# Kernel tuning notes

Hardware: AMD Instinct MI355X
Metric: run time of the kernel (lower is better)

The kernel has to match this reference:

```python
import jax, jax.numpy as jnp
import numpy as np

IN_FEATURES = 1024
OUT_FEATURES = 256
NUM_KNOTS = 10
SPLINE_ORDER = 3
NUM_BASIS = NUM_KNOTS + SPLINE_ORDER  # 13
EPS = 1e-8


def setup_inputs() -> dict:
    key = jax.random.key(0)
    k1, k2 = jax.random.split(key)
    x = jax.random.normal(k1, (8192, IN_FEATURES), dtype=jnp.float32)
    spline_coeffs = jax.random.normal(
        k2, (OUT_FEATURES, IN_FEATURES, NUM_BASIS), dtype=jnp.float32) * 0.1
    knots = jnp.linspace(-1.0, 1.0, NUM_KNOTS + 2 * SPLINE_ORDER, dtype=jnp.float32)
    return {"x": x, "spline_coeffs": spline_coeffs, "knots": knots}


def _basis_functions(x, knots):
    # x: (B, I) already tanh-normalized; returns (B, I, NUM_BASIS)
    xc = jnp.clip(x, -1.0, 1.0)[..., None]          # (B, I, 1)
    left = knots[:NUM_BASIS - 1]                     # (nb-1,)
    center = knots[1:NUM_BASIS]                      # (nb-1,)
    right = knots[2:NUM_BASIS + 1]                   # (nb-1,)  (i+2 < len(knots) always)
    mask_l = (xc >= left) & (xc < center)
    mask_r = (xc >= center) & (xc < right)
    up = mask_l.astype(xc.dtype) * (xc - left) / (center - left + EPS)
    down = mask_r.astype(xc.dtype) * (right - xc) / (right - center + EPS)
    b = up + down                                    # (B, I, nb-1)
    # last basis column is never written in the original loop -> zeros
    return jnp.pad(b, ((0, 0), (0, 0), (0, 1)))


def reference(x, spline_coeffs, knots):
    x_norm = jnp.tanh(x)
    basis = _basis_functions(x_norm, knots)          # (B, I, K)
    # output[b, j] = sum_i sum_k basis[b, i, k] * coeffs[j, i, k]
    return jnp.einsum('bik,jik->bj', basis, spline_coeffs)
```

## Files before the change

### kernel.cpp

```cpp
#include <hip/hip_runtime.h>
#include <cstdint>
#include <cstddef>


typedef _Float16 half2_v __attribute__((ext_vector_type(2)));
typedef __fp16  fp16x2  __attribute__((ext_vector_type(2)));
typedef _Float16 f16x8 __attribute__((ext_vector_type(8)));
typedef float f32x4 __attribute__((ext_vector_type(4)));

__device__ __forceinline__ half2_v u32_as_h2(uint32_t u) {
  union { uint32_t u; half2_v h; } c; c.u = u; return c.h;
}
__device__ __forceinline__ uint32_t h2_as_u32(half2_v h) {
  union { uint32_t u; half2_v h; } c; c.h = h; return c.u;
}
__device__ __forceinline__ half2_v cvt_pk_h2(float a, float b) {
  union { fp16x2 f; half2_v h; } c;
  c.f = __builtin_amdgcn_cvt_pkrtz(a, b);
  return c.h;
}
__device__ __forceinline__ float dot2f(half2_v a, half2_v b, float c) {
#if __has_builtin(__builtin_amdgcn_fdot2)
  return __builtin_amdgcn_fdot2(a, b, c, false);
#else
  return c + (float)a[0] * (float)b[0] + (float)a[1] * (float)b[1];
#endif
}
__device__ __forceinline__ uint16_t f16_bits(float v) {
  union { _Float16 h; uint16_t u; } c; c.h = (_Float16)v; return c.u;
}

__device__ __forceinline__ float fast_tanhf(float v) {
  const float e = __expf(2.0f * v);
  return 1.0f - 2.0f / (e + 1.0f);
}

#define KSTEP 0.13333333333333333f
#define KINV  7.49999943750004f
__device__ __forceinline__ void kan_weights(float xin, float& w0, float& w1, int& lo) {
  float xc = fast_tanhf(xin);
  xc = fminf(fmaxf(xc, -1.0f), 1.0f);
  int m = (int)((xc + 1.0f) * 7.5f);
  m = min(max(m, 0), 14);
  const float k0 = fmaf((float)m, KSTEP, -1.0f);
  const float up = (xc - k0) * KINV;
  const float dn = (k0 + KSTEP - xc) * KINV;
  w0 = (m == 0) ? up : ((m <= 12) ? dn : 0.0f);
  w1 = (m >= 1 && m <= 11) ? up : 0.0f;
  lo = min(max(m - 1, 0), 11);
}

__device__ __forceinline__ void load_lds16(const void* g, void* l) {
  __builtin_amdgcn_global_load_lds((const __attribute__((address_space(1))) void*)g,
                                   (__attribute__((address_space(3))) void*)l, 16, 0, 0);
}

#define GMM 8192
#define GNN 256
#define KI  16
#define GK2 (1024 * KI)
#define KSPL2 8
#define IPER (1024 / KSPL2)
#define BM2 128
#define BN2 256
#define NGRAN 64
#define NBODY 16

__global__ __launch_bounds__(256)
void kan_prep_B2(const float* __restrict__ coef, uint32_t* __restrict__ B2,
                 float4* __restrict__ outz) {
  const int tid = blockIdx.x * 256 + threadIdx.x;
  const float* cp = coef + (size_t)tid * 13;
  uint32_t w[8];
#pragma unroll
  for (int q = 0; q < 6; ++q) w[q] = h2_as_u32(cvt_pk_h2(cp[2 * q], cp[2 * q + 1]));
  w[6] = 0u; w[7] = 0u;
  uint4* p = (uint4*)(B2 + (size_t)tid * 8);
  p[0] = make_uint4(w[0], w[1], w[2], w[3]);
  p[1] = make_uint4(w[4], w[5], w[6], w[7]);
  const float4 z = make_float4(0.f, 0.f, 0.f, 0.f);
  outz[tid] = z;
  outz[tid + 262144] = z;
}

__global__ __launch_bounds__(512, 4)
void kan_gemm10(const float* __restrict__ x, const _Float16* __restrict__ B2,
                float* __restrict__ out) {
  __shared__ __align__(16) char Bs[4][16384];
  __shared__ __align__(16) char As[2][8192];
  char* BsP = (char*)Bs;
  char* AsP = (char*)As;

  const int t    = threadIdx.x;
  const int lane = t & 63;
  const int wv   = t >> 6;
  const int wm   = (wv & 1) * 64;
  const int wn   = (wv >> 1) * 64;
  const int fr   = lane & 15;
  const int fq   = lane >> 4;
  const int m0   = blockIdx.z * BM2;
  const int i00  = blockIdx.x * IPER;

  const int fr_swz = (((wm >> 2) + (fr >> 2)) & 1) * 16;
  const int a_base = (wm + fr) * 32 + (((fq & 1) * 16) ^ fr_swz) + (fq >> 1) * 4096;
  const int b_base = (wn + fr) * 64 + ((fq ^ (fr & 3)) * 16);

  f32x4 acc[4][4];
#pragma unroll
  for (int a = 0; a < 4; ++a)
#pragma unroll
    for (int b = 0; b < 4; ++b) acc[a][b] = (f32x4){0.f, 0.f, 0.f, 0.f};

  const int srow0 = t >> 2, sc0 = t & 3;
  const int srow1 = 128 + (t >> 2);
  const _Float16* sp0 = B2 + (size_t)srow0 * GK2 + (size_t)i00 * KI
                        + ((sc0 ^ (srow0 & 3)) * 8);
  const _Float16* sp1 = B2 + (size_t)srow1 * GK2 + (size_t)i00 * KI
                        + ((sc0 ^ (srow1 & 3)) * 8);
  const int xrow   = (t >> 1) & 127;
  const int parity = t & 1;
  const int i_off  = (t >> 8) & 1;
  const float* xptr = x + (size_t)(m0 + xrow) * 1024 + i00 + 2 * parity + i_off;
  const int exp_off = (i_off * 128 + xrow) * 32;
  const int p_swz   = ((xrow >> 2) & 1) * 16;

  auto expand1 = [&](int aw, float xv) {
    float w0, w1; int lo;
    kan_weights(xv, w0, w1, lo);
    const uint32_t wp  = (uint32_t)f16_bits(w0) | ((uint32_t)f16_bits(w1) << 16);
    const uint32_t wlo = (lo & 1) ? (wp << 16) : wp;
    const uint32_t whi = (lo & 1) ? (wp >> 16) : 0u;
    const int w = lo >> 1;
    char* rb = AsP + aw + exp_off;
    *(uint4*)(rb + p_swz)        = make_uint4(0u, 0u, 0u, 0u);
    *(uint4*)(rb + (p_swz ^ 16)) = make_uint4(0u, 0u, 0u, 0u);
    *(uint32_t*)(rb + (((w + 1) * 4) ^ p_swz)) = whi;
    *(uint32_t*)(rb + ((w * 4) ^ p_swz))       = wlo;
  };

  float xa, xb, xn1, xn2;

  xa = xptr[0];
  xb = xptr[4];
  load_lds16(sp0, BsP + 0 + t * 16);
  load_lds16(sp1, BsP + 0 + 8192 + t * 16);
  sp0 += 32; sp1 += 32;
  load_lds16(sp0, BsP + 16384 + t * 16);
  load_lds16(sp1, BsP + 16384 + 8192 + t * 16);
  sp0 += 32; sp1 += 32;
  if (parity == 0) expand1(0, xa);
  asm volatile("s_waitcnt vmcnt(2) lgkmcnt(0)" ::: "memory");
  __builtin_amdgcn_s_barrier();
  __builtin_amdgcn_sched_barrier(0);

#define MFMA16(RS)                                                            \
  __builtin_amdgcn_s_setprio(1);                                              \
  _Pragma("unroll")                                                           \
  for (int ni = 0; ni < 4; ++ni) {                                            \
    const f16x8 bf = *(const f16x8*)(BsP + (RS) + b_base + ni * 1024);        \
    acc[0][ni] = __builtin_amdgcn_mfma_f32_16x16x32_f16(af0, bf, acc[0][ni], 0, 0, 0); \
    acc[1][ni] = __builtin_amdgcn_mfma_f32_16x16x32_f16(af1, bf, acc[1][ni], 0, 0, 0); \
    acc[2][ni] = __builtin_amdgcn_mfma_f32_16x16x32_f16(af2, bf, acc[2][ni], 0, 0, 0); \
    acc[3][ni] = __builtin_amdgcn_mfma_f32_16x16x32_f16(af3, bf, acc[3][ni], 0, 0, 0); \
  }                                                                           \
  __builtin_amdgcn_s_setprio(0);

#define GRAN(P, XV, ADV, XLOAD)                                               \
  {                                                                           \
    f16x8 af0 = *(const f16x8*)(AsP + ((P) & 1) * 8192 + a_base);             \
    f16x8 af1 = *(const f16x8*)(AsP + ((P) & 1) * 8192 + a_base + 512);       \
    f16x8 af2 = *(const f16x8*)(AsP + ((P) & 1) * 8192 + a_base + 1024);      \
    f16x8 af3 = *(const f16x8*)(AsP + ((P) & 1) * 8192 + a_base + 1536);      \
    load_lds16(sp0, BsP + (((P) + 2) & 3) * 16384 + t * 16);                  \
    load_lds16(sp1, BsP + (((P) + 2) & 3) * 16384 + 8192 + t * 16);           \
    sp0 += (ADV); sp1 += (ADV);                                               \
    XLOAD                                                                     \
    if (parity == (((P) + 1) & 1)) expand1((((P) + 1) & 1) * 8192, XV);       \
    asm volatile("s_waitcnt vmcnt(3) lgkmcnt(0)" ::: "memory");               \
    __builtin_amdgcn_s_barrier();                                             \
    __builtin_amdgcn_sched_barrier(0);                                        \
    MFMA16((P) * 16384)                                                       \
  }

  for (int itw = 0; itw < NBODY; ++itw) {
    const int g0 = 4 * itw;
    const int adv0 = (g0 + 3 <= NGRAN - 1) ? 32 : 0;
    const int adv1 = (g0 + 4 <= NGRAN - 1) ? 32 : 0;
    const int adv2 = (g0 + 5 <= NGRAN - 1) ? 32 : 0;
    const int adv3 = (g0 + 6 <= NGRAN - 1) ? 32 : 0;
    int xw1 = 2 * itw + 2; if (xw1 > 31) xw1 = 31;
    int xw2 = 2 * itw + 3; if (xw2 > 31) xw2 = 31;

    GRAN(0, xa, adv0, { xn1 = xptr[4 * xw1]; })
    GRAN(1, xb, adv1, { })
    GRAN(2, xb, adv2, { xn2 = xptr[4 * xw2]; })
    GRAN(3, xn1, adv3, { })

    xa = xn1; xb = xn2;
  }
#undef GRAN
#undef MFMA16

#pragma unroll
  for (int q = 0; q < 4; ++q) {
    const int gr = m0 + wm + q * 16 + fq * 4;
#pragma unroll
    for (int ni = 0; ni < 4; ++ni) {
      const int gc = wn + ni * 16 + fr;
#pragma unroll
      for (int r = 0; r < 4; ++r)
        atomicAdd(&out[(size_t)(gr + r) * GNN + gc], acc[q][ni][r]);
    }
  }
}

#define TI 8
#define BT 256
#define JT 32
#define ISPL 2
#define IRANGE (1024 / ISPL)

__global__ __launch_bounds__(256)
void kan_dot2(const float* __restrict__ x, const float* __restrict__ coef,
              float* __restrict__ out) {
  __shared__ uint32_t Plds[TI * 12 * JT];
  const int t    = threadIdx.x;
  const int b    = blockIdx.x * BT + t;
  const int j0   = blockIdx.y * JT;
  const int cbeg = blockIdx.z * (IRANGE / TI);

  float acc[JT];
#pragma unroll
  for (int q = 0; q < JT; ++q) acc[q] = 0.0f;

  const int s_jj   = t & 31;
  const int s_iloc = t >> 5;

  for (int c = cbeg; c < cbeg + IRANGE / TI; ++c) {
    const int i0 = c * TI;
    __syncthreads();
    {
      const float* cp0 = coef + ((size_t)(j0 + s_jj) * 1024 + (i0 + s_iloc)) * 13;
      float cv[13];
#pragma unroll
      for (int s = 0; s < 13; ++s) cv[s] = cp0[s];
#pragma unroll
      for (int r = 0; r < 12; ++r) {
        half2_v h; h[0] = (_Float16)cv[r]; h[1] = (_Float16)cv[r + 1];
        const int slot = ((s_jj >> 2) + r) & 7;
        Plds[(s_iloc * 12 + r) * 32 + slot * 4 + (s_jj & 3)] = h2_as_u32(h);
      }
    }
    uint32_t wr[TI]; int lor[TI];
    {
      const float* xr = x + (size_t)b * 1024 + i0;
      const float4 xa = *(const float4*)(xr);
      const float4 xb = *(const float4*)(xr + 4);
      const float xv[TI] = {xa.x, xa.y, xa.z, xa.w, xb.x, xb.y, xb.z, xb.w};
#pragma unroll
      for (int q = 0; q < TI; ++q) {
        float w0, w1; int lo;
        kan_weights(xv[q], w0, w1, lo);
        wr[q] = (uint32_t)f16_bits(w0) | ((uint32_t)f16_bits(w1) << 16);
        lor[q] = lo;
      }
    }
    __syncthreads();

    const uint4* P4 = (const uint4*)Plds;
#pragma unroll
    for (int ii = 0; ii < TI; ++ii) {
      const half2_v hw = u32_as_h2(wr[ii]);
      const int lo = lor[ii];
      const int base = (ii * 12 + lo) * 8;
#pragma unroll
      for (int g = 0; g < 8; ++g) {
        const uint4 v = P4[base + ((g + lo) & 7)];
        acc[4 * g + 0] = dot2f(hw, u32_as_h2(v.x), acc[4 * g + 0]);
        acc[4 * g + 1] = dot2f(hw, u32_as_h2(v.y), acc[4 * g + 1]);
        acc[4 * g + 2] = dot2f(hw, u32_as_h2(v.z), acc[4 * g + 2]);
        acc[4 * g + 3] = dot2f(hw, u32_as_h2(v.w), acc[4 * g + 3]);
      }
    }
  }

  float* orow = out + (size_t)b * 256 + j0;
#pragma unroll
  for (int q = 0; q < JT; ++q) atomicAdd(orow + q, acc[q]);
}

extern "C" void kernel_launch(void* const* d_in, const int* in_sizes, int n_in,
                              void* d_out, int out_size, void* d_ws, size_t ws_size,
                              hipStream_t stream) {
  const float* x     = (const float*)d_in[0];
  const float* coef  = (const float*)d_in[1];
  float* out = (float*)d_out;

  const size_t nB2 = (size_t)GNN * GK2;
  if (ws_size >= nB2 * 2) {
    _Float16* B2 = (_Float16*)d_ws;
    kan_prep_B2<<<(int)((size_t)GNN * 1024 / 256), 256, 0, stream>>>(
        coef, (uint32_t*)B2, (float4*)out);
    dim3 grid(KSPL2, 1, GMM / BM2);
    kan_gemm10<<<grid, 512, 0, stream>>>(x, B2, out);
  } else {
    (void)hipMemsetAsync(out, 0, (size_t)out_size * sizeof(float), stream);
    dim3 grid(8192 / BT, 256 / JT, ISPL);
    kan_dot2<<<grid, 256, 0, stream>>>(x, coef, out);
  }
}
```

Baseline: 193.2 us.

## Pack spline basis to 12 halves per feature, cutting GEMM K padding

```diff
diff --git a/kernel.cpp b/kernel.cpp
--- a/kernel.cpp
+++ b/kernel.cpp
@@ -57,37 +57,39 @@
 
 #define GMM 8192
 #define GNN 256
-#define KI  16
+#define KI  12
 #define GK2 (1024 * KI)
 #define KSPL2 8
 #define IPER (1024 / KSPL2)
 #define BM2 128
 #define BN2 256
-#define NGRAN 64
-#define NBODY 16
+#define NSG 16
+#define NSTEP 48
+#define AS_STRIDE 208
+#define AS_SG (128 * AS_STRIDE)
 
 __global__ __launch_bounds__(256)
 void kan_prep_B2(const float* __restrict__ coef, uint32_t* __restrict__ B2,
                  float4* __restrict__ outz) {
   const int tid = blockIdx.x * 256 + threadIdx.x;
   const float* cp = coef + (size_t)tid * 13;
-  uint32_t w[8];
+  uint32_t w[6];
 #pragma unroll
   for (int q = 0; q < 6; ++q) w[q] = h2_as_u32(cvt_pk_h2(cp[2 * q], cp[2 * q + 1]));
-  w[6] = 0u; w[7] = 0u;
-  uint4* p = (uint4*)(B2 + (size_t)tid * 8);
-  p[0] = make_uint4(w[0], w[1], w[2], w[3]);
-  p[1] = make_uint4(w[4], w[5], w[6], w[7]);
+  uint2* p = (uint2*)(B2 + (size_t)tid * 6);
+  p[0] = make_uint2(w[0], w[1]);
+  p[1] = make_uint2(w[2], w[3]);
+  p[2] = make_uint2(w[4], w[5]);
   const float4 z = make_float4(0.f, 0.f, 0.f, 0.f);
   outz[tid] = z;
   outz[tid + 262144] = z;
 }
 
-__global__ __launch_bounds__(512, 4)
-void kan_gemm10(const float* __restrict__ x, const _Float16* __restrict__ B2,
+__global__ __launch_bounds__(512, 2)
+void kan_gemm12(const float* __restrict__ x, const _Float16* __restrict__ B2,
                 float* __restrict__ out) {
   __shared__ __align__(16) char Bs[4][16384];
-  __shared__ __align__(16) char As[2][8192];
+  __shared__ __align__(16) char As[2][AS_SG];
   char* BsP = (char*)Bs;
   char* AsP = (char*)As;
 
@@ -101,8 +103,7 @@
   const int m0   = blockIdx.z * BM2;
   const int i00  = blockIdx.x * IPER;
 
-  const int fr_swz = (((wm >> 2) + (fr >> 2)) & 1) * 16;
-  const int a_base = (wm + fr) * 32 + (((fq & 1) * 16) ^ fr_swz) + (fq >> 1) * 4096;
+  const int a_base = (wm + fr) * AS_STRIDE + fq * 16;
   const int b_base = (wn + fr) * 64 + ((fq ^ (fr & 3)) * 16);
 
   f32x4 acc[4][4];
@@ -117,89 +118,101 @@
                         + ((sc0 ^ (srow0 & 3)) * 8);
   const _Float16* sp1 = B2 + (size_t)srow1 * GK2 + (size_t)i00 * KI
                         + ((sc0 ^ (srow1 & 3)) * 8);
-  const int xrow   = (t >> 1) & 127;
-  const int parity = t & 1;
-  const int i_off  = (t >> 8) & 1;
-  const float* xptr = x + (size_t)(m0 + xrow) * 1024 + i00 + 2 * parity + i_off;
-  const int exp_off = (i_off * 128 + xrow) * 32;
-  const int p_swz   = ((xrow >> 2) & 1) * 16;
-
-  auto expand1 = [&](int aw, float xv) {
+
+  const int xrow  = t & 127;
+  const int i_loc = t >> 7;
+  const float* xptr = x + (size_t)(m0 + xrow) * 1024 + i00 + i_loc;
+
+  auto expand1 = [&](int dst, float xv, int il) {
     float w0, w1; int lo;
     kan_weights(xv, w0, w1, lo);
     const uint32_t wp  = (uint32_t)f16_bits(w0) | ((uint32_t)f16_bits(w1) << 16);
     const uint32_t wlo = (lo & 1) ? (wp << 16) : wp;
     const uint32_t whi = (lo & 1) ? (wp >> 16) : 0u;
-    const int w = lo >> 1;
-    char* rb = AsP + aw + exp_off;
-    *(uint4*)(rb + p_swz)        = make_uint4(0u, 0u, 0u, 0u);
-    *(uint4*)(rb + (p_swz ^ 16)) = make_uint4(0u, 0u, 0u, 0u);
-    *(uint32_t*)(rb + (((w + 1) * 4) ^ p_swz)) = whi;
-    *(uint32_t*)(rb + ((w * 4) ^ p_swz))       = wlo;
+    const int w   = lo >> 1;
+    const int wn1 = (w + 1 > 5) ? 5 : (w + 1);
+    char* rb = AsP + dst + xrow * AS_STRIDE + il * 24;
+    if ((il & 1) == 0) {
+      *(uint4*)(rb)      = make_uint4(0u, 0u, 0u, 0u);
+      *(uint2*)(rb + 16) = make_uint2(0u, 0u);
+    } else {
+      *(uint2*)(rb)      = make_uint2(0u, 0u);
+      *(uint4*)(rb + 8)  = make_uint4(0u, 0u, 0u, 0u);
+    }
+    *(uint32_t*)(rb + wn1 * 4) = whi;
+    *(uint32_t*)(rb + w * 4)   = wlo;
   };
 
-  float xa, xb, xn1, xn2;
-
-  xa = xptr[0];
-  xb = xptr[4];
-  load_lds16(sp0, BsP + 0 + t * 16);
-  load_lds16(sp1, BsP + 0 + 8192 + t * 16);
-  sp0 += 32; sp1 += 32;
-  load_lds16(sp0, BsP + 16384 + t * 16);
-  load_lds16(sp1, BsP + 16384 + 8192 + t * 16);
-  sp0 += 32; sp1 += 32;
-  if (parity == 0) expand1(0, xa);
+  float cxa, cxb, nxa = 0.f, nxb = 0.f;
+
+  {
+    const float exa = xptr[0];
+    const float exb = xptr[4];
+    load_lds16(sp0, BsP + t * 16);
+    load_lds16(sp1, BsP + 8192 + t * 16);
+    sp0 += 32; sp1 += 32;
+    load_lds16(sp0, BsP + 16384 + t * 16);
+    load_lds16(sp1, BsP + 16384 + 8192 + t * 16);
+    sp0 += 32; sp1 += 32;
+    expand1(0, exa, i_loc);
+    expand1(0, exb, i_loc + 4);
+    cxa = xptr[8];
+    cxb = xptr[12];
+  }
   asm volatile("s_waitcnt vmcnt(2) lgkmcnt(0)" ::: "memory");
   __builtin_amdgcn_s_barrier();
   __builtin_amdgcn_sched_barrier(0);
 
-#define MFMA16(RS)                                                            \
-  __builtin_amdgcn_s_setprio(1);                                              \
-  _Pragma("unroll")                                                           \
-  for (int ni = 0; ni < 4; ++ni) {                                            \
-    const f16x8 bf = *(const f16x8*)(BsP + (RS) + b_base + ni * 1024);        \
-    acc[0][ni] = __builtin_amdgcn_mfma_f32_16x16x32_f16(af0, bf, acc[0][ni], 0, 0, 0); \
-    acc[1][ni] = __builtin_amdgcn_mfma_f32_16x16x32_f16(af1, bf, acc[1][ni], 0, 0, 0); \
-    acc[2][ni] = __builtin_amdgcn_mfma_f32_16x16x32_f16(af2, bf, acc[2][ni], 0, 0, 0); \
-    acc[3][ni] = __builtin_amdgcn_mfma_f32_16x16x32_f16(af3, bf, acc[3][ni], 0, 0, 0); \
-  }                                                                           \
-  __builtin_amdgcn_s_setprio(0);
-
-#define GRAN(P, XV, ADV, XLOAD)                                               \
+#define GRANP(U, PH, XPF)                                                     \
   {                                                                           \
-    f16x8 af0 = *(const f16x8*)(AsP + ((P) & 1) * 8192 + a_base);             \
-    f16x8 af1 = *(const f16x8*)(AsP + ((P) & 1) * 8192 + a_base + 512);       \
-    f16x8 af2 = *(const f16x8*)(AsP + ((P) & 1) * 8192 + a_base + 1024);      \
-    f16x8 af3 = *(const f16x8*)(AsP + ((P) & 1) * 8192 + a_base + 1536);      \
-    load_lds16(sp0, BsP + (((P) + 2) & 3) * 16384 + t * 16);                  \
-    load_lds16(sp1, BsP + (((P) + 2) & 3) * 16384 + 8192 + t * 16);           \
-    sp0 += (ADV); sp1 += (ADV);                                               \
-    XLOAD                                                                     \
-    if (parity == (((P) + 1) & 1)) expand1((((P) + 1) & 1) * 8192, XV);       \
+    const int g = 12 * B + 3 * (U) + (PH);                                    \
+    const char* Asrc = AsP + ((U) & 1) * AS_SG;                               \
+    f16x8 af0 = *(const f16x8*)(Asrc + a_base + (PH) * 64);                   \
+    f16x8 af1 = *(const f16x8*)(Asrc + a_base + (PH) * 64 + 16 * AS_STRIDE);  \
+    f16x8 af2 = *(const f16x8*)(Asrc + a_base + (PH) * 64 + 32 * AS_STRIDE);  \
+    f16x8 af3 = *(const f16x8*)(Asrc + a_base + (PH) * 64 + 48 * AS_STRIDE);  \
+    load_lds16(sp0, BsP + ((3 * (U) + (PH) + 2) & 3) * 16384 + t * 16);       \
+    load_lds16(sp1, BsP + ((3 * (U) + (PH) + 2) & 3) * 16384 + 8192 + t * 16);\
+    { const int adv = (g + 3 <= NSTEP - 1) ? 32 : 0; sp0 += adv; sp1 += adv; }\
+    XPF                                                                       \
+    if ((PH) == 0 && (4 * B + (U)) < NSG - 1)                                 \
+      expand1((((U) + 1) & 1) * AS_SG, cxa, i_loc);                           \
+    if ((PH) == 1 && (4 * B + (U)) < NSG - 1)                                 \
+      expand1((((U) + 1) & 1) * AS_SG, cxb, i_loc + 4);                       \
     asm volatile("s_waitcnt vmcnt(3) lgkmcnt(0)" ::: "memory");               \
     __builtin_amdgcn_s_barrier();                                             \
     __builtin_amdgcn_sched_barrier(0);                                        \
-    MFMA16((P) * 16384)                                                       \
-  }
-
-  for (int itw = 0; itw < NBODY; ++itw) {
-    const int g0 = 4 * itw;
-    const int adv0 = (g0 + 3 <= NGRAN - 1) ? 32 : 0;
-    const int adv1 = (g0 + 4 <= NGRAN - 1) ? 32 : 0;
-    const int adv2 = (g0 + 5 <= NGRAN - 1) ? 32 : 0;
-    const int adv3 = (g0 + 6 <= NGRAN - 1) ? 32 : 0;
-    int xw1 = 2 * itw + 2; if (xw1 > 31) xw1 = 31;
-    int xw2 = 2 * itw + 3; if (xw2 > 31) xw2 = 31;
-
-    GRAN(0, xa, adv0, { xn1 = xptr[4 * xw1]; })
-    GRAN(1, xb, adv1, { })
-    GRAN(2, xb, adv2, { xn2 = xptr[4 * xw2]; })
-    GRAN(3, xn1, adv3, { })
-
-    xa = xn1; xb = xn2;
-  }
-#undef GRAN
-#undef MFMA16
+    __builtin_amdgcn_s_setprio(1);                                            \
+    _Pragma("unroll")                                                         \
+    for (int ni = 0; ni < 4; ++ni) {                                          \
+      const f16x8 bf = *(const f16x8*)(BsP + ((3 * (U) + (PH)) & 3) * 16384   \
+                                       + b_base + ni * 1024);                 \
+      acc[0][ni] = __builtin_amdgcn_mfma_f32_16x16x32_f16(af0, bf, acc[0][ni], 0, 0, 0); \
+      acc[1][ni] = __builtin_amdgcn_mfma_f32_16x16x32_f16(af1, bf, acc[1][ni], 0, 0, 0); \
+      acc[2][ni] = __builtin_amdgcn_mfma_f32_16x16x32_f16(af2, bf, acc[2][ni], 0, 0, 0); \
+      acc[3][ni] = __builtin_amdgcn_mfma_f32_16x16x32_f16(af3, bf, acc[3][ni], 0, 0, 0); \
+    }                                                                         \
+    __builtin_amdgcn_s_setprio(0);                                            \
+  }
+
+#define SGBODY(U)                                                             \
+  {                                                                           \
+    const int sgp = 4 * B + (U) + 2;                                          \
+    const int sgn = (sgp < NSG) ? sgp : (NSG - 1);                            \
+    GRANP(U, 0, { nxa = xptr[8 * sgn]; })                                     \
+    GRANP(U, 1, { })                                                          \
+    GRANP(U, 2, { nxb = xptr[8 * sgn + 4]; })                                 \
+    cxa = nxa; cxb = nxb;                                                     \
+  }
+
+  for (int B = 0; B < 4; ++B) {
+    SGBODY(0)
+    SGBODY(1)
+    SGBODY(2)
+    SGBODY(3)
+  }
+#undef SGBODY
+#undef GRANP
 
 #pragma unroll
   for (int q = 0; q < 4; ++q) {
@@ -302,7 +315,7 @@
     kan_prep_B2<<<(int)((size_t)GNN * 1024 / 256), 256, 0, stream>>>(
         coef, (uint32_t*)B2, (float4*)out);
     dim3 grid(KSPL2, 1, GMM / BM2);
-    kan_gemm10<<<grid, 512, 0, stream>>>(x, B2, out);
+    kan_gemm12<<<grid, 512, 0, stream>>>(x, B2, out);
   } else {
     (void)hipMemsetAsync(out, 0, (size_t)out_size * sizeof(float), stream);
     dim3 grid(8192 / BT, 256 / JT, ISPL);
```

Result: no change. 196.4 us (+1.6%).
